# Performance work log

Hardware: AMD Instinct MI355X
Metric: run time of the kernel (lower is better)

The kernel has to match this reference:

```python
import jax, jax.numpy as jnp
import numpy as np

N = 100000   # nodes
E = 2500000  # edges (before self-loops)
G = 64       # graphs in the batch


def _glorot(key, fi, fo):
    return jax.random.normal(key, (fi, fo), jnp.float32) * jnp.sqrt(2.0 / (fi + fo))


def setup_inputs() -> dict:
    key = jax.random.key(0)
    ks = jax.random.split(key, 8)
    x = jax.random.normal(ks[0], (N, 3), jnp.float32)
    edge_index = jax.random.randint(ks[1], (2, E), 0, N)
    batch = jnp.sort(jax.random.randint(ks[2], (N,), 0, G))
    return dict(
        x=x, edge_index=edge_index, batch=batch,
        W1=_glorot(ks[3], 3, 16),  b1=jnp.zeros((16,), jnp.float32),
        W2=_glorot(ks[4], 16, 32), b2=jnp.zeros((32,), jnp.float32),
        W3=_glorot(ks[5], 32, 16), b3=jnp.zeros((16,), jnp.float32),
        W4=_glorot(ks[6], 16, 2),  b4=jnp.zeros((2,), jnp.float32),
    )


def reference(x, edge_index, batch, W1, b1, W2, b2, W3, b3, W4, b4):
    # PyG GCNConv: add self-loops, sym-normalize by deg^{-1/2}, gather->scatter-add.
    loops = jnp.arange(N)
    src = jnp.concatenate([edge_index[0], loops])  # [E+N]
    dst = jnp.concatenate([edge_index[1], loops])
    deg = jax.ops.segment_sum(jnp.ones_like(dst, jnp.float32), dst, num_segments=N)
    dinv = jax.lax.rsqrt(jnp.maximum(deg, 1.0))  # deg >= 1 due to self-loops
    norm = (dinv[src] * dinv[dst])[:, None]      # [E+N, 1]

    def gcn_conv(h, W, b):
        h = h @ W                                  # [N, out]
        msg = h[src] * norm                        # gather + edge scaling
        agg = jax.ops.segment_sum(msg, dst, num_segments=N)  # scatter-add
        return agg + b

    h = jax.nn.relu(gcn_conv(x, W1, b1))
    h = jax.nn.relu(gcn_conv(h, W2, b2))
    h = jax.nn.relu(gcn_conv(h, W3, b3))
    # F.dropout with training=False (module in eval) is identity
    h = gcn_conv(h, W4, b4)                        # [N, 2]

    # global_mean_pool over graph ids
    sums = jax.ops.segment_sum(h, batch, num_segments=G)
    cnts = jax.ops.segment_sum(jnp.ones((N,), h.dtype), batch, num_segments=G)
    pooled = sums / jnp.maximum(cnts, 1.0)[:, None]  # [G, 2]
    return jax.nn.log_softmax(pooled, axis=1)
```

## Files before the change

### kernel.cpp

```cpp
#include <hip/hip_runtime.h>
#include <hip/hip_fp16.h>
#include <cmath>

static constexpr int NN = 100000;
static constexpr int NE = 2500000;
static constexpr int NG = 64;
static constexpr int NBUCK = (NN + 255) / 256;
static constexpr int CHUNK = 4096;
static constexpr int NCHUNK = (NE + CHUNK - 1) / CHUNK;
static constexpr int CAP = 8192;

union H8 { float4 f4; __half2 h2[4]; };
union H4 { float2 f2; __half2 h2[2]; };

__device__ inline void unpack_add(float* a, float4 r) {
    H8 u; u.f4 = r;
#pragma unroll
    for (int k = 0; k < 4; ++k) { float2 f = __half22float2(u.h2[k]); a[2*k] += f.x; a[2*k+1] += f.y; }
}
__device__ inline unsigned pack2(float f0, float f1) {
    __half2 h = __floats2half2_rn(f0, f1);
    return *reinterpret_cast<unsigned*>(&h);
}

__global__ void p1_hist(const int* __restrict__ dst, int* __restrict__ Ht) {
    __shared__ int hist[NBUCK];
    int t = threadIdx.x, c = blockIdx.x;
    for (int i = t; i < NBUCK; i += 256) hist[i] = 0;
    __syncthreads();
    int e0 = c * CHUNK, e1 = min(e0 + CHUNK, NE);
    for (int e = e0 + t; e < e1; e += 256) atomicAdd(&hist[dst[e] >> 8], 1);
    __syncthreads();
    for (int b = t; b < NBUCK; b += 256) Ht[(size_t)b * NCHUNK + c] = hist[b];
}

__global__ void p2_scan(int* __restrict__ Ht, int* __restrict__ count,
                        float* __restrict__ pooled3) {
    __shared__ int s[256];
    int b = blockIdx.x, t = threadIdx.x;
    if (b == 0 && t < NG * 3) pooled3[t] = 0.0f;
    int* row = Ht + (size_t)b * NCHUNK;
    int carry = 0;
    for (int seg = 0; seg < 3; ++seg) {
        int idx = seg * 256 + t;
        int v = (idx < NCHUNK) ? row[idx] : 0;
        __syncthreads();
        s[t] = v;
        __syncthreads();
#pragma unroll
        for (int off = 1; off < 256; off <<= 1) {
            int y = (t >= off) ? s[t - off] : 0;
            __syncthreads();
            s[t] += y;
            __syncthreads();
        }
        int incl = s[t];
        int segtot = s[255];
        if (idx < NCHUNK) row[idx] = incl - v + carry;
        carry += segtot;
    }
    if (t == 0) count[b] = carry;
}

__global__ void p3_scatter(const int* __restrict__ src, const int* __restrict__ dst,
                           const int* __restrict__ Ht, int* __restrict__ staging) {
    __shared__ int cur[NBUCK];
    int t = threadIdx.x, bid = blockIdx.x;
    int x = bid & 7, o = bid >> 3;
    int len = 76 + (x < 3 ? 1 : 0);
    if (o >= len) return;
    int c = x * 76 + min(x, 3) + o;
    for (int b = t; b < NBUCK; b += 256) cur[b] = Ht[(size_t)b * NCHUNK + c];
    __syncthreads();
    int e0 = c * CHUNK, e1 = min(e0 + CHUNK, NE);
    for (int e = e0 + t; e < e1; e += 256) {
        int d = dst[e];
        int b = d >> 8;
        int r = atomicAdd(&cur[b], 1);
        staging[((size_t)b << 13) + r] = src[e] | ((d & 255) << 17);
    }
}

__global__ void csr_build_kernel(const int* __restrict__ staging, const int* __restrict__ count,
                                 const float* __restrict__ x,
                                 unsigned* __restrict__ rsd, float* __restrict__ dinv,
                                 int* __restrict__ csr_src, float2* __restrict__ xsh) {
    __shared__ int hist[256];
    __shared__ int scn[256];
    __shared__ int cur[256];
    int b = blockIdx.x, t = threadIdx.x;
    int cnt = count[b];
    int base = b << 13;
    hist[t] = 0;
    __syncthreads();
    const int* st = staging + ((size_t)b << 13);
    for (int i = t; i < cnt; i += 256) atomicAdd(&hist[st[i] >> 17], 1);
    __syncthreads();
    int h = hist[t];
    scn[t] = h; __syncthreads();
#pragma unroll
    for (int off = 1; off < 256; off <<= 1) {
        int y = (t >= off) ? scn[t - off] : 0;
        __syncthreads();
        scn[t] += y;
        __syncthreads();
    }
    int ex = scn[t] - h;
    int v = (b << 8) + t;
    if (v < NN) {
        float dv = rsqrtf((float)h + 1.0f);
        rsd[v]  = (unsigned)(base + ex) | ((unsigned)h << 23);
        dinv[v] = dv;
        H4 u;
        u.h2[0] = __floats2half2_rn(x[v * 3] * dv, x[v * 3 + 1] * dv);
        u.h2[1] = __floats2half2_rn(x[v * 3 + 2] * dv, 0.0f);
        xsh[v] = u.f2;
    }
    cur[t] = ex;
    __syncthreads();
    for (int i = t; i < cnt; i += 256) {
        int p = st[i];
        int r = atomicAdd(&cur[p >> 17], 1);
        csr_src[base + r] = p & 0x1FFFF;
    }
}

__global__ void __launch_bounds__(256) agg3t1_kernel(const float2* __restrict__ xsh,
        const int* __restrict__ csr, const unsigned* __restrict__ rsd,
        const float* __restrict__ dinv, const float* __restrict__ W1,
        const float* __restrict__ b1, unsigned* __restrict__ g2h) {
    __shared__ float sW1[48], sb1[16];
    int t = threadIdx.x;
    if (t < 48) sW1[t] = W1[t];
    if (t < 16) sb1[t] = b1[t];
    __syncthreads();
    int tid = blockIdx.x * 256 + t;
    int v = tid >> 3, p = tid & 7;
    if (v >= NN) return;
    float a0 = 0.0f, a1 = 0.0f, a2 = 0.0f;
    if (p == 0) {
        H4 u; u.f2 = xsh[v];
        float2 f0 = __half22float2(u.h2[0]), f1 = __half22float2(u.h2[1]);
        a0 = f0.x; a1 = f0.y; a2 = f1.x;
    }
    unsigned rd = rsd[v];
    int s0 = rd & 0x7FFFFF, cnt = rd >> 23;
    for (int j = p; j < cnt; j += 8) {
        H4 u; u.f2 = xsh[csr[s0 + j]];
        float2 f0 = __half22float2(u.h2[0]), f1 = __half22float2(u.h2[1]);
        a0 += f0.x; a1 += f0.y; a2 += f1.x;
    }
    a0 += __shfl_xor(a0, 1); a1 += __shfl_xor(a1, 1); a2 += __shfl_xor(a2, 1);
    a0 += __shfl_xor(a0, 2); a1 += __shfl_xor(a1, 2); a2 += __shfl_xor(a2, 2);
    a0 += __shfl_xor(a0, 4); a1 += __shfl_xor(a1, 4); a2 += __shfl_xor(a2, 4);
    float dv = dinv[v];
    a0 *= dv; a1 *= dv; a2 *= dv;
    float f[2];
#pragma unroll
    for (int k = 0; k < 2; ++k) {
        int fo = p * 2 + k;
        float g = fmaf(a0, sW1[fo], fmaf(a1, sW1[16 + fo], fmaf(a2, sW1[32 + fo], sb1[fo])));
        f[k] = fmaxf(g, 0.0f) * dv;
    }
    g2h[v * 8 + p] = pack2(f[0], f[1]);
}

__global__ void __launch_bounds__(256) agg16mid_kernel(const float4* __restrict__ g2h,
        const int* __restrict__ csr, const unsigned* __restrict__ rsd,
        const float* __restrict__ dinv, const float* __restrict__ W2,
        const float* __restrict__ b2, const float* __restrict__ W3,
        unsigned* __restrict__ g3h) {
    __shared__ float sW2[512], sW3[512], sb2[32];
    int t = threadIdx.x;
    for (int i = t; i < 512; i += 256) { sW2[i] = W2[i]; sW3[i] = W3[i]; }
    if (t < 32) sb2[t] = b2[t];
    __syncthreads();
    int tid = blockIdx.x * 256 + t;
    int v = tid >> 3, p = tid & 7;
    if (v >= NN) return;
    float a[16];
#pragma unroll
    for (int f = 0; f < 16; ++f) a[f] = 0.0f;
    if (p == 0) { unpack_add(a, g2h[v * 2]); unpack_add(a + 8, g2h[v * 2 + 1]); }
    unsigned rd = rsd[v];
    int s0 = rd & 0x7FFFFF, cnt = rd >> 23;
    for (int j = p; j < cnt; j += 8) {
        int s = csr[s0 + j];
        unpack_add(a,     g2h[s * 2]);
        unpack_add(a + 8, g2h[s * 2 + 1]);
    }
#pragma unroll
    for (int f = 0; f < 16; ++f) a[f] += __shfl_xor(a[f], 1);
#pragma unroll
    for (int f = 0; f < 16; ++f) a[f] += __shfl_xor(a[f], 2);
#pragma unroll
    for (int f = 0; f < 16; ++f) a[f] += __shfl_xor(a[f], 4);
    float dv = dinv[v];
#pragma unroll
    for (int f = 0; f < 16; ++f) a[f] *= dv;
    float h2p[4];
#pragma unroll
    for (int k = 0; k < 4; ++k) {
        int fo = p * 4 + k;
        float s = sb2[fo];
#pragma unroll
        for (int fi = 0; fi < 16; ++fi) s = fmaf(a[fi], sW2[fi * 32 + fo], s);
        h2p[k] = fmaxf(s, 0.0f);
    }
    float po[16];
#pragma unroll
    for (int fo = 0; fo < 16; ++fo) {
        float s = h2p[0] * sW3[(p * 4 + 0) * 16 + fo];
        s = fmaf(h2p[1], sW3[(p * 4 + 1) * 16 + fo], s);
        s = fmaf(h2p[2], sW3[(p * 4 + 2) * 16 + fo], s);
        s = fmaf(h2p[3], sW3[(p * 4 + 3) * 16 + fo], s);
        po[fo] = s;
    }
#pragma unroll
    for (int f = 0; f < 16; ++f) po[f] += __shfl_xor(po[f], 1);
#pragma unroll
    for (int f = 0; f < 16; ++f) po[f] += __shfl_xor(po[f], 2);
#pragma unroll
    for (int f = 0; f < 16; ++f) po[f] += __shfl_xor(po[f], 4);
    g3h[v * 8 + p] = pack2(po[p * 2] * dv, po[p * 2 + 1] * dv);
}

__global__ void __launch_bounds__(256) agg16t4_kernel(const float4* __restrict__ g3h,
        const int* __restrict__ csr, const unsigned* __restrict__ rsd,
        const float* __restrict__ dinv, const float* __restrict__ b3,
        const float* __restrict__ W4, float2* __restrict__ g4) {
    __shared__ float sb3[16], sW4[32];
    int t = threadIdx.x;
    if (t < 16) sb3[t] = b3[t];
    if (t < 32) sW4[t] = W4[t];
    __syncthreads();
    int tid = blockIdx.x * 256 + t;
    int v = tid >> 3, p = tid & 7;
    if (v >= NN) return;
    float a[16];
#pragma unroll
    for (int f = 0; f < 16; ++f) a[f] = 0.0f;
    if (p == 0) { unpack_add(a, g3h[v * 2]); unpack_add(a + 8, g3h[v * 2 + 1]); }
    unsigned rd = rsd[v];
    int s0 = rd & 0x7FFFFF, cnt = rd >> 23;
    for (int j = p; j < cnt; j += 8) {
        int s = csr[s0 + j];
        unpack_add(a,     g3h[s * 2]);
        unpack_add(a + 8, g3h[s * 2 + 1]);
    }
#pragma unroll
    for (int f = 0; f < 16; ++f) a[f] += __shfl_xor(a[f], 1);
#pragma unroll
    for (int f = 0; f < 16; ++f) a[f] += __shfl_xor(a[f], 2);
#pragma unroll
    for (int f = 0; f < 16; ++f) a[f] += __shfl_xor(a[f], 4);
    float dv = dinv[v];
    int f0 = p * 2, f1 = p * 2 + 1;
    float h3a = fmaxf(fmaf(a[f0], dv, sb3[f0]), 0.0f);
    float h3b = fmaxf(fmaf(a[f1], dv, sb3[f1]), 0.0f);
    float o0 = fmaf(h3a, sW4[f0 * 2 + 0], h3b * sW4[f1 * 2 + 0]);
    float o1 = fmaf(h3a, sW4[f0 * 2 + 1], h3b * sW4[f1 * 2 + 1]);
    o0 += __shfl_xor(o0, 1); o1 += __shfl_xor(o1, 1);
    o0 += __shfl_xor(o0, 2); o1 += __shfl_xor(o1, 2);
    o0 += __shfl_xor(o0, 4); o1 += __shfl_xor(o1, 4);
    if (p == 0) g4[v] = make_float2(o0 * dv, o1 * dv);
}

__global__ void __launch_bounds__(256) agg2pool_kernel(const float2* __restrict__ g4,
        const int* __restrict__ csr, const unsigned* __restrict__ rsd,
        const float* __restrict__ dinv, const float* __restrict__ b4,
        const int* __restrict__ batch, float* __restrict__ pooled3) {
    __shared__ float spool[NG * 3];
    int t = threadIdx.x;
    for (int i = t; i < NG * 3; i += 256) spool[i] = 0.0f;
    __syncthreads();
    int tid = blockIdx.x * 256 + t;
    int v = tid >> 3, p = tid & 7;
    if (v < NN) {
        float a0 = 0.0f, a1 = 0.0f;
        if (p == 0) { float2 s = g4[v]; a0 = s.x; a1 = s.y; }
        unsigned rd = rsd[v];
        int s0 = rd & 0x7FFFFF, cnt = rd >> 23;
        for (int j = p; j < cnt; j += 8) {
            float2 q = g4[csr[s0 + j]];
            a0 += q.x; a1 += q.y;
        }
        a0 += __shfl_xor(a0, 1); a1 += __shfl_xor(a1, 1);
        a0 += __shfl_xor(a0, 2); a1 += __shfl_xor(a1, 2);
        a0 += __shfl_xor(a0, 4); a1 += __shfl_xor(a1, 4);
        if (p == 0) {
            float dv = dinv[v];
            float o0 = fmaf(a0, dv, b4[0]);
            float o1 = fmaf(a1, dv, b4[1]);
            int gi = batch[v];
            atomicAdd(&spool[gi * 3 + 0], o0);
            atomicAdd(&spool[gi * 3 + 1], o1);
            atomicAdd(&spool[gi * 3 + 2], 1.0f);
        }
    }
    __syncthreads();
    for (int i = t; i < NG * 3; i += 256)
        if (spool[i] != 0.0f) atomicAdd(&pooled3[i], spool[i]);
}

__global__ void lsm_kernel(const float* __restrict__ pooled3, float* __restrict__ out) {
    int g = threadIdx.x;
    if (g < NG) {
        float c = fmaxf(pooled3[g * 3 + 2], 1.0f);
        float a = pooled3[g * 3 + 0] / c;
        float b = pooled3[g * 3 + 1] / c;
        float m = fmaxf(a, b);
        float lse = m + logf(expf(a - m) + expf(b - m));
        out[g * 2 + 0] = a - lse;
        out[g * 2 + 1] = b - lse;
    }
}

extern "C" void kernel_launch(void* const* d_in, const int* in_sizes, int n_in,
                              void* d_out, int out_size, void* d_ws, size_t ws_size,
                              hipStream_t stream) {
    (void)in_sizes; (void)n_in; (void)out_size; (void)ws_size;

    const float* x   = (const float*)d_in[0];
    const int*   ei  = (const int*)d_in[1];
    const int*   bat = (const int*)d_in[2];
    const float* W1  = (const float*)d_in[3];
    const float* b1  = (const float*)d_in[4];
    const float* W2  = (const float*)d_in[5];
    const float* b2  = (const float*)d_in[6];
    const float* W3  = (const float*)d_in[7];
    const float* b3  = (const float*)d_in[8];
    const float* W4  = (const float*)d_in[9];
    const float* b4  = (const float*)d_in[10];
    float* out = (float*)d_out;

    const int* src = ei;
    const int* dst = ei + NE;

    char* w = (char*)d_ws;
    int*      Ht      = (int*)w;      w += ((size_t)NBUCK * NCHUNK * 4 + 15) & ~15ull;
    int*      count   = (int*)w;      w += ((size_t)NBUCK * 4 + 15) & ~15ull;
    int*      staging = (int*)w;      w += (size_t)NBUCK * CAP * 4;
    int*      csr_src = (int*)w;      w += (size_t)NBUCK * CAP * 4;
    unsigned* rsd     = (unsigned*)w; w += (size_t)NN * 4;
    float*    dinv    = (float*)w;    w += (size_t)NN * 4;
    float2*   xsh     = (float2*)w;   w += (size_t)NN * 8;
    unsigned* g2h     = (unsigned*)w; w += (size_t)NN * 32;
    unsigned* g3h     = (unsigned*)w; w += (size_t)NN * 32;
    float2*   g4      = (float2*)w;   w += (size_t)NN * 8;
    float*    pooled3 = (float*)w;    w += NG * 3 * 4;

    const int gN8 = (NN * 8 + 255) / 256;

    p1_hist<<<NCHUNK, 256, 0, stream>>>(dst, Ht);
    p2_scan<<<NBUCK, 256, 0, stream>>>(Ht, count, pooled3);
    p3_scatter<<<616, 256, 0, stream>>>(src, dst, Ht, staging);
    csr_build_kernel<<<NBUCK, 256, 0, stream>>>(staging, count, x, rsd, dinv, csr_src, xsh);

    agg3t1_kernel<<<gN8, 256, 0, stream>>>(xsh, csr_src, rsd, dinv, W1, b1, g2h);
    agg16mid_kernel<<<gN8, 256, 0, stream>>>((const float4*)g2h, csr_src, rsd, dinv, W2, b2,
                                             W3, g3h);
    agg16t4_kernel<<<gN8, 256, 0, stream>>>((const float4*)g3h, csr_src, rsd, dinv, b3, W4, g4);
    agg2pool_kernel<<<gN8, 256, 0, stream>>>(g4, csr_src, rsd, dinv, b4, bat, pooled3);

    lsm_kernel<<<1, 64, 0, stream>>>(pooled3, out);
}
```

Baseline: 162.4 us.

## Unroll gather loops by two and compute full layer-2 transform per lane

Each CSR gather loop in the four aggregation kernels now handles two neighbors per iteration, so more independent loads are in flight and memory latency is better hidden. The middle kernel also stops splitting the 16x32 and 32x16 transforms across the 8 lanes and replacing that with 48 shuffle reductions. Instead each lane computes all 32 hidden features redundantly, then only its own two outputs. This removes the shuffles but multiplies per-lane FMA work and register use, which may cut occupancy.

```diff
diff --git a/kernel.cpp b/kernel.cpp
--- a/kernel.cpp
+++ b/kernel.cpp
@@ -144,8 +144,19 @@
         a0 = f0.x; a1 = f0.y; a2 = f1.x;
     }
     unsigned rd = rsd[v];
-    int s0 = rd & 0x7FFFFF, cnt = rd >> 23;
-    for (int j = p; j < cnt; j += 8) {
+    int s0 = rd & 0x7FFFFF, cnt = (int)(rd >> 23);
+    int j = p;
+    for (; j + 8 < cnt; j += 16) {
+        int s1 = csr[s0 + j];
+        int s2 = csr[s0 + j + 8];
+        H4 u1; u1.f2 = xsh[s1];
+        H4 u2; u2.f2 = xsh[s2];
+        float2 f0 = __half22float2(u1.h2[0]), f1 = __half22float2(u1.h2[1]);
+        a0 += f0.x; a1 += f0.y; a2 += f1.x;
+        f0 = __half22float2(u2.h2[0]); f1 = __half22float2(u2.h2[1]);
+        a0 += f0.x; a1 += f0.y; a2 += f1.x;
+    }
+    if (j < cnt) {
         H4 u; u.f2 = xsh[csr[s0 + j]];
         float2 f0 = __half22float2(u.h2[0]), f1 = __half22float2(u.h2[1]);
         a0 += f0.x; a1 += f0.y; a2 += f1.x;
@@ -181,13 +192,22 @@
     float a[16];
 #pragma unroll
     for (int f = 0; f < 16; ++f) a[f] = 0.0f;
-    if (p == 0) { unpack_add(a, g2h[v * 2]); unpack_add(a + 8, g2h[v * 2 + 1]); }
+    if (p == 0) { unpack_add(a, g2h[(size_t)v * 2]); unpack_add(a + 8, g2h[(size_t)v * 2 + 1]); }
     unsigned rd = rsd[v];
-    int s0 = rd & 0x7FFFFF, cnt = rd >> 23;
-    for (int j = p; j < cnt; j += 8) {
-        int s = csr[s0 + j];
-        unpack_add(a,     g2h[s * 2]);
-        unpack_add(a + 8, g2h[s * 2 + 1]);
+    int s0 = rd & 0x7FFFFF, cnt = (int)(rd >> 23);
+    int j = p;
+    for (; j + 8 < cnt; j += 16) {
+        int s1 = csr[s0 + j];
+        int s2 = csr[s0 + j + 8];
+        float4 xa = g2h[(size_t)s1 * 2], xb = g2h[(size_t)s1 * 2 + 1];
+        float4 ya = g2h[(size_t)s2 * 2], yb = g2h[(size_t)s2 * 2 + 1];
+        unpack_add(a, xa); unpack_add(a + 8, xb);
+        unpack_add(a, ya); unpack_add(a + 8, yb);
+    }
+    if (j < cnt) {
+        int s1 = csr[s0 + j];
+        float4 xa = g2h[(size_t)s1 * 2], xb = g2h[(size_t)s1 * 2 + 1];
+        unpack_add(a, xa); unpack_add(a + 8, xb);
     }
 #pragma unroll
     for (int f = 0; f < 16; ++f) a[f] += __shfl_xor(a[f], 1);
@@ -198,31 +218,24 @@
     float dv = dinv[v];
 #pragma unroll
     for (int f = 0; f < 16; ++f) a[f] *= dv;
-    float h2p[4];
-#pragma unroll
-    for (int k = 0; k < 4; ++k) {
-        int fo = p * 4 + k;
+    float h2[32];
+#pragma unroll
+    for (int fo = 0; fo < 32; ++fo) {
         float s = sb2[fo];
 #pragma unroll
         for (int fi = 0; fi < 16; ++fi) s = fmaf(a[fi], sW2[fi * 32 + fo], s);
-        h2p[k] = fmaxf(s, 0.0f);
-    }
-    float po[16];
-#pragma unroll
-    for (int fo = 0; fo < 16; ++fo) {
-        float s = h2p[0] * sW3[(p * 4 + 0) * 16 + fo];
-        s = fmaf(h2p[1], sW3[(p * 4 + 1) * 16 + fo], s);
-        s = fmaf(h2p[2], sW3[(p * 4 + 2) * 16 + fo], s);
-        s = fmaf(h2p[3], sW3[(p * 4 + 3) * 16 + fo], s);
-        po[fo] = s;
-    }
-#pragma unroll
-    for (int f = 0; f < 16; ++f) po[f] += __shfl_xor(po[f], 1);
-#pragma unroll
-    for (int f = 0; f < 16; ++f) po[f] += __shfl_xor(po[f], 2);
-#pragma unroll
-    for (int f = 0; f < 16; ++f) po[f] += __shfl_xor(po[f], 4);
-    g3h[v * 8 + p] = pack2(po[p * 2] * dv, po[p * 2 + 1] * dv);
+        h2[fo] = fmaxf(s, 0.0f);
+    }
+    float o[2];
+#pragma unroll
+    for (int k = 0; k < 2; ++k) {
+        int fo = p * 2 + k;
+        float s = 0.0f;
+#pragma unroll
+        for (int fi = 0; fi < 32; ++fi) s = fmaf(h2[fi], sW3[fi * 16 + fo], s);
+        o[k] = s * dv;
+    }
+    g3h[v * 8 + p] = pack2(o[0], o[1]);
 }
 
 __global__ void __launch_bounds__(256) agg16t4_kernel(const float4* __restrict__ g3h,
@@ -240,13 +253,22 @@
     float a[16];
 #pragma unroll
     for (int f = 0; f < 16; ++f) a[f] = 0.0f;
-    if (p == 0) { unpack_add(a, g3h[v * 2]); unpack_add(a + 8, g3h[v * 2 + 1]); }
+    if (p == 0) { unpack_add(a, g3h[(size_t)v * 2]); unpack_add(a + 8, g3h[(size_t)v * 2 + 1]); }
     unsigned rd = rsd[v];
-    int s0 = rd & 0x7FFFFF, cnt = rd >> 23;
-    for (int j = p; j < cnt; j += 8) {
-        int s = csr[s0 + j];
-        unpack_add(a,     g3h[s * 2]);
-        unpack_add(a + 8, g3h[s * 2 + 1]);
+    int s0 = rd & 0x7FFFFF, cnt = (int)(rd >> 23);
+    int j = p;
+    for (; j + 8 < cnt; j += 16) {
+        int s1 = csr[s0 + j];
+        int s2 = csr[s0 + j + 8];
+        float4 xa = g3h[(size_t)s1 * 2], xb = g3h[(size_t)s1 * 2 + 1];
+        float4 ya = g3h[(size_t)s2 * 2], yb = g3h[(size_t)s2 * 2 + 1];
+        unpack_add(a, xa); unpack_add(a + 8, xb);
+        unpack_add(a, ya); unpack_add(a + 8, yb);
+    }
+    if (j < cnt) {
+        int s1 = csr[s0 + j];
+        float4 xa = g3h[(size_t)s1 * 2], xb = g3h[(size_t)s1 * 2 + 1];
+        unpack_add(a, xa); unpack_add(a + 8, xb);
     }
 #pragma unroll
     for (int f = 0; f < 16; ++f) a[f] += __shfl_xor(a[f], 1);
@@ -280,8 +302,14 @@
         float a0 = 0.0f, a1 = 0.0f;
         if (p == 0) { float2 s = g4[v]; a0 = s.x; a1 = s.y; }
         unsigned rd = rsd[v];
-        int s0 = rd & 0x7FFFFF, cnt = rd >> 23;
-        for (int j = p; j < cnt; j += 8) {
+        int s0 = rd & 0x7FFFFF, cnt = (int)(rd >> 23);
+        int j = p;
+        for (; j + 8 < cnt; j += 16) {
+            float2 q1 = g4[csr[s0 + j]];
+            float2 q2 = g4[csr[s0 + j + 8]];
+            a0 += q1.x + q2.x; a1 += q1.y + q2.y;
+        }
+        if (j < cnt) {
             float2 q = g4[csr[s0 + j]];
             a0 += q.x; a1 += q.y;
         }
```

New measurement: 153.9 us. -5.2%, faster.
